# Performance work log

Measured on AMD Instinct MI355X. Metric: run time of the kernel, lower is better.

## Reference

```python
import jax, jax.numpy as jnp
import numpy as np

D, H, L, P, NQ, B, DFF = 256, 8, 4, 4, 900, 4, 1024
SHAPES = [(128, 128), (64, 64), (32, 32), (16, 16)]
S = sum(h * w for h, w in SHAPES)  # 21760
HD = D // H


def setup_inputs() -> dict:
    key = jax.random.key(0)
    ks = iter(jax.random.split(key, 32))
    r = lambda sh, s=1.0: jax.random.normal(next(ks), sh, jnp.float32) * s
    return dict(
        tgt=r((B, NQ, D)),
        query_pos=r((B, NQ, D)),
        reference_points=jax.random.uniform(next(ks), (B, NQ, L, 2), jnp.float32),
        memory=r((B, S, D)),
        in_proj_w=r((D, 3 * D), 0.02), in_proj_b=jnp.zeros(3 * D, jnp.float32),
        out_proj_w=r((D, D), 0.02), out_proj_b=jnp.zeros(D, jnp.float32),
        ln1_g=jnp.ones(D, jnp.float32), ln1_b=jnp.zeros(D, jnp.float32),
        ln2_g=jnp.ones(D, jnp.float32), ln2_b=jnp.zeros(D, jnp.float32),
        ln3_g=jnp.ones(D, jnp.float32), ln3_b=jnp.zeros(D, jnp.float32),
        vproj_w=r((D, D), 0.02), vproj_b=jnp.zeros(D, jnp.float32),
        off_w=r((D, H * L * P * 2), 0.02), off_b=r((H * L * P * 2,), 0.5),
        aw_w=r((D, H * L * P), 0.02), aw_b=jnp.zeros(H * L * P, jnp.float32),
        oproj_w=r((D, D), 0.02), oproj_b=jnp.zeros(D, jnp.float32),
        lin1_w=r((D, DFF), 0.02), lin1_b=jnp.zeros(DFF, jnp.float32),
        lin2_w=r((DFF, D), 0.02), lin2_b=jnp.zeros(D, jnp.float32),
        spatial_shapes=np.array(SHAPES, np.int32),
        mem_mask=jnp.zeros((B, S), bool),
    )


def _ln(x, g, b):
    m = jnp.mean(x, -1, keepdims=True)
    v = jnp.mean((x - m) ** 2, -1, keepdims=True)
    return (x - m) * jax.lax.rsqrt(v + 1e-5) * g + b


def reference(tgt, query_pos, reference_points, memory,
              in_proj_w, in_proj_b, out_proj_w, out_proj_b,
              ln1_g, ln1_b, ln2_g, ln2_b, ln3_g, ln3_b,
              vproj_w, vproj_b, off_w, off_b, aw_w, aw_b, oproj_w, oproj_b,
              lin1_w, lin1_b, lin2_w, lin2_b, spatial_shapes, mem_mask):
    shapes = np.asarray(spatial_shapes)  # static level shapes

    # ---- self attention (nn.MultiheadAttention, q=k=tgt+pos, v=tgt) ----
    qp = tgt + query_pos
    q = qp @ in_proj_w[:, :D] + in_proj_b[:D]
    k = qp @ in_proj_w[:, D:2 * D] + in_proj_b[D:2 * D]
    v = tgt @ in_proj_w[:, 2 * D:] + in_proj_b[2 * D:]
    split = lambda x: x.reshape(B, NQ, H, HD).transpose(0, 2, 1, 3)
    qh, kh, vh = split(q), split(k), split(v)
    att = jax.nn.softmax(jnp.einsum('bhqd,bhkd->bhqk', qh, kh) / np.sqrt(HD).astype(np.float32), -1)
    sa = jnp.einsum('bhqk,bhkd->bhqd', att, vh).transpose(0, 2, 1, 3).reshape(B, NQ, D)
    tgt = _ln(tgt + sa @ out_proj_w + out_proj_b, ln2_g, ln2_b)

    # ---- MSDeformAttn cross attention ----
    query = tgt + query_pos
    value = memory @ vproj_w + vproj_b
    value = jnp.where(mem_mask[..., None], 0.0, value).reshape(B, S, H, HD)
    off = (query @ off_w + off_b).reshape(B, NQ, H, L, P, 2)
    aw = jax.nn.softmax((query @ aw_w + aw_b).reshape(B, NQ, H, L * P), -1).reshape(B, NQ, H, L, P)
    # offset normalizer is (W_l, H_l)
    normalizer = jnp.stack([jnp.asarray(shapes[:, 1]), jnp.asarray(shapes[:, 0])], -1).astype(jnp.float32)
    loc = reference_points[:, :, None, :, None, :] + off / normalizer[None, None, None, :, None, :]

    acc = jnp.zeros((B, NQ, H, HD), tgt.dtype)
    start = 0
    bidx = jnp.arange(B)[:, None, None, None]
    hidx = jnp.arange(H)[None, None, :, None]
    for l in range(L):
        Hl, Wl = int(shapes[l, 0]), int(shapes[l, 1])
        vf = value[:, start:start + Hl * Wl]  # [B, Hl*Wl, H, HD]
        # grid_sample align_corners=False, zero padding: pixel = loc*size - 0.5
        x = loc[:, :, :, l, :, 0] * Wl - 0.5  # [B,NQ,H,P]
        y = loc[:, :, :, l, :, 1] * Hl - 0.5
        x0 = jnp.floor(x); y0 = jnp.floor(y)
        wx = x - x0; wy = y - y0
        x0i = x0.astype(jnp.int32); y0i = y0.astype(jnp.int32)

        def gather(xi, yi):
            valid = (xi >= 0) & (xi < Wl) & (yi >= 0) & (yi < Hl)
            idx = jnp.clip(yi, 0, Hl - 1) * Wl + jnp.clip(xi, 0, Wl - 1)
            g = vf[bidx, idx, hidx]  # [B,NQ,H,P,HD]
            return jnp.where(valid[..., None], g, 0.0)

        samp = (gather(x0i, y0i) * ((1 - wx) * (1 - wy))[..., None]
                + gather(x0i + 1, y0i) * (wx * (1 - wy))[..., None]
                + gather(x0i, y0i + 1) * ((1 - wx) * wy)[..., None]
                + gather(x0i + 1, y0i + 1) * (wx * wy)[..., None])
        acc = acc + (samp * aw[:, :, :, l, :, None]).sum(3)
        start += Hl * Wl

    ca = acc.reshape(B, NQ, D) @ oproj_w + oproj_b
    tgt = _ln(tgt + ca, ln1_g, ln1_b)

    # ---- FFN ----
    ff = jax.nn.relu(tgt @ lin1_w + lin1_b) @ lin2_w + lin2_b
    return _ln(tgt + ff, ln3_g, ln3_b)
```

## Files before the change

### kernel.cpp

```cpp
#include <hip/hip_runtime.h>
#include <hip/hip_bf16.h>

typedef __attribute__((ext_vector_type(8))) short bf16x8;
typedef __attribute__((ext_vector_type(4))) short bf16x4;
typedef __attribute__((ext_vector_type(4))) float f32x4;

#define DEV static __device__ __forceinline__

constexpr int Bc = 4, NQc = 900, Hc = 8, Sc = 21760;
constexpr int M1 = Bc * NQc;
constexpr int NQT = (NQc + 63) / 64;
constexpr int QT16 = (NQc + 15) / 16;
constexpr int QKo = Bc * Hc * 960 * 32;

DEV short f2bf(float f) {
  union { __hip_bfloat16 h; short s; } u;
  u.h = __float2bfloat16(f);
  return u.s;
}
DEV float bf2f(short s) {
  union { short s; __hip_bfloat16 h; } u;
  u.s = s;
  return __bfloat162float(u.h);
}

DEV void pack_body(const float* W, short* Wt, int K, int N, int t) {
  int n = t % N;
  int k4 = (t / N) * 4;
  bf16x4 o;
  o[0] = f2bf(W[(size_t)(k4 + 0) * N + n]);
  o[1] = f2bf(W[(size_t)(k4 + 1) * N + n]);
  o[2] = f2bf(W[(size_t)(k4 + 2) * N + n]);
  o[3] = f2bf(W[(size_t)(k4 + 3) * N + n]);
  *(bf16x4*)&Wt[((size_t)(k4 >> 5) * N + n) * 32 + (k4 & 31)] = o;
}

__global__ __launch_bounds__(256) void pack_all_k(
    const float* w0, short* t0, const float* w1, short* t1,
    const float* w2, short* t2, const float* w3, short* t3,
    const float* w4, short* t4, const float* w5, short* t5) {
  int t = blockIdx.x * 256 + threadIdx.x;
  if (t < 49152) pack_body(w0, t0, 256, 768, t);
  else if (t < 65536) pack_body(w1, t1, 256, 256, t - 49152);
  else if (t < 81920) pack_body(w2, t2, 256, 256, t - 65536);
  else if (t < 98304) pack_body(w3, t3, 256, 256, t - 81920);
  else if (t < 163840) pack_body(w4, t4, 256, 1024, t - 98304);
  else pack_body(w5, t5, 1024, 256, t - 163840);
}

template <int MODE, int ACT, int MT>
__global__ __launch_bounds__(256) void gemmv_k(
    const float* __restrict__ A, const float* __restrict__ A2,
    const short* __restrict__ Wt, const float* __restrict__ bias,
    void* __restrict__ Cv, float* __restrict__ C2, int M, int N, int K,
    const unsigned char* __restrict__ rowmask, const float* __restrict__ g,
    const float* __restrict__ beta, const float* __restrict__ resid,
    const float* __restrict__ qpos, float* __restrict__ out2) {
  constexpr int IT = MT / 16;
  __shared__ short As[MT * 40];
  __shared__ short Ws[256 * 40];
  const int nb = N >> 8;
  const int mb = blockIdx.x / nb, bn = blockIdx.x - mb * nb;
  const int tid = threadIdx.x;
  const int lane = tid & 63, wave = tid >> 6;
  const int l16 = lane & 15, quad = lane >> 4;
  const int sr = (MT == 64) ? (tid >> 2) : (tid >> 3);
  const int sk = (MT == 64) ? ((tid & 3) * 8) : ((tid & 7) * 4);
  const int arow = mb * MT + sr;
  const bool aval = arow < M;
  const bool useA2 = (MODE == 4) ? (bn < 2) : (A2 != nullptr);
  const float* ap = A + (size_t)arow * K + sk;
  const float* ap2 = (A2 ? A2 : A) + (size_t)arow * K + sk;
  const short* wp = Wt + (size_t)(bn * 256 + tid) * 32;
  const size_t wstep = (size_t)N * 32;
  const int KT = K >> 5;

  f32x4 acc[IT][4] = {};
  float4 pa0[2] = {}, pa1[2] = {};
  bf16x8 pw[2][4];

  auto loadA = [&](int s, int it) {
    if (aval) {
      const float* p = ap + it * 32;
      pa0[s] = *(const float4*)p;
      if constexpr (MT == 64) pa1[s] = *(const float4*)(p + 4);
      if (useA2) {
        const float* p2 = ap2 + it * 32;
        float4 q0 = *(const float4*)p2;
        pa0[s].x += q0.x; pa0[s].y += q0.y; pa0[s].z += q0.z; pa0[s].w += q0.w;
        if constexpr (MT == 64) {
          float4 q1 = *(const float4*)(p2 + 4);
          pa1[s].x += q1.x; pa1[s].y += q1.y; pa1[s].z += q1.z; pa1[s].w += q1.w;
        }
      }
    }
  };
  auto loadW = [&](int s, int it) {
    const short* p = wp + (size_t)it * wstep;
    pw[s][0] = *(const bf16x8*)(p + 0);
    pw[s][1] = *(const bf16x8*)(p + 8);
    pw[s][2] = *(const bf16x8*)(p + 16);
    pw[s][3] = *(const bf16x8*)(p + 24);
  };
  auto stage = [&](int s) {
    if constexpr (MT == 64) {
      bf16x8 t;
      t[0] = f2bf(pa0[s].x); t[1] = f2bf(pa0[s].y); t[2] = f2bf(pa0[s].z); t[3] = f2bf(pa0[s].w);
      t[4] = f2bf(pa1[s].x); t[5] = f2bf(pa1[s].y); t[6] = f2bf(pa1[s].z); t[7] = f2bf(pa1[s].w);
      *(bf16x8*)&As[sr * 40 + sk] = t;
    } else {
      bf16x4 t;
      t[0] = f2bf(pa0[s].x); t[1] = f2bf(pa0[s].y); t[2] = f2bf(pa0[s].z); t[3] = f2bf(pa0[s].w);
      *(bf16x4*)&As[sr * 40 + sk] = t;
    }
    short* wd = &Ws[tid * 40];
    *(bf16x8*)(wd + 0) = pw[s][0];
    *(bf16x8*)(wd + 8) = pw[s][1];
    *(bf16x8*)(wd + 16) = pw[s][2];
    *(bf16x8*)(wd + 24) = pw[s][3];
  };
  auto compute = [&]() {
    bf16x8 af[IT], bfr[4];
#pragma unroll
    for (int i = 0; i < IT; i++)
      af[i] = *(const bf16x8*)&As[(i * 16 + l16) * 40 + quad * 8];
#pragma unroll
    for (int j = 0; j < 4; j++)
      bfr[j] = *(const bf16x8*)&Ws[(wave * 64 + j * 16 + l16) * 40 + quad * 8];
#pragma unroll
    for (int i = 0; i < IT; i++)
#pragma unroll
      for (int j = 0; j < 4; j++)
        acc[i][j] = __builtin_amdgcn_mfma_f32_16x16x32_bf16(af[i], bfr[j], acc[i][j], 0, 0, 0);
  };

  loadA(0, 0); loadW(0, 0);
  loadA(1, 1); loadW(1, 1);
  for (int it = 0; it < KT; it += 2) {
    stage(0);
    __syncthreads();
    if (it + 2 < KT) { loadA(0, it + 2); loadW(0, it + 2); }
    compute();
    __syncthreads();
    stage(1);
    __syncthreads();
    if (it + 3 < KT) { loadA(1, it + 3); loadW(1, it + 3); }
    compute();
    __syncthreads();
  }

  if constexpr (MODE == 4) {
    short* base = (short*)Cv;
#pragma unroll
    for (int i = 0; i < IT; i++)
#pragma unroll
      for (int r = 0; r < 4; r++) {
        const int m = mb * MT + i * 16 + quad * 4 + r;
        if (m >= M) continue;
        const int b = m / NQc, q = m - b * NQc;
#pragma unroll
        for (int j = 0; j < 4; j++) {
          const int cl = wave * 64 + j * 16 + l16;
          const float v = acc[i][j][r] + bias[bn * 256 + cl];
          const int h = cl >> 5, ch = cl & 31;
          if (bn == 0) {
            base[((size_t)(b * 8 + h) * 960 + q) * 32 + ch] =
                f2bf(v * 0.17677669529663687f);
          } else if (bn == 1) {
            base[QKo + ((size_t)(b * 8 + h) * 960 + q) * 32 + ch] = f2bf(v);
          } else {
            base[2 * QKo + ((((size_t)(b * 8 + h) * 15 + (q >> 6)) * 32 + ch) * 64 + (q & 63))] = f2bf(v);
          }
        }
      }
  } else if constexpr (MODE == 0) {
#pragma unroll
    for (int i = 0; i < IT; i++)
#pragma unroll
      for (int j = 0; j < 4; j++) {
        const int cl = wave * 64 + j * 16 + l16;
        const int col = bn * 256 + cl;
        const float bb = bias[col];
#pragma unroll
        for (int r = 0; r < 4; r++) {
          const int m = mb * MT + i * 16 + quad * 4 + r;
          if (m < M) {
            float v = acc[i][j][r] + bb;
            if (ACT == 1) v = fmaxf(v, 0.f);
            ((float*)Cv)[(size_t)m * N + col] = v;
          }
        }
      }
  } else {
#pragma unroll
    for (int j = 0; j < 4; j++) {
      const int cl = wave * 64 + j * 16 + l16;
      const float bb = bias[cl];
#pragma unroll
      for (int i = 0; i < IT; i++)
#pragma unroll
        for (int r = 0; r < 4; r++) {
          const int m = mb * MT + i * 16 + quad * 4 + r;
          const float rs = (m < M) ? resid[(size_t)m * 256 + cl] : 0.f;
          acc[i][j][r] += bb + rs;
        }
    }
    float2* pr = (float2*)As;
#pragma unroll
    for (int i = 0; i < IT; i++)
#pragma unroll
      for (int r = 0; r < 4; r++) {
        float s = 0.f, q = 0.f;
#pragma unroll
        for (int j = 0; j < 4; j++) {
          s += acc[i][j][r];
          q += acc[i][j][r] * acc[i][j][r];
        }
#pragma unroll
        for (int d = 1; d < 16; d <<= 1) {
          s += __shfl_xor(s, d);
          q += __shfl_xor(q, d);
        }
        if (l16 == 0) pr[(i * 16 + quad * 4 + r) * 4 + wave] = make_float2(s, q);
      }
    __syncthreads();
#pragma unroll
    for (int i = 0; i < IT; i++)
#pragma unroll
      for (int r = 0; r < 4; r++) {
        const int ml = i * 16 + quad * 4 + r;
        float2 p0 = pr[ml * 4 + 0], p1 = pr[ml * 4 + 1];
        float2 p2 = pr[ml * 4 + 2], p3 = pr[ml * 4 + 3];
        const float sum = p0.x + p1.x + p2.x + p3.x;
        const float sq = p0.y + p1.y + p2.y + p3.y;
        const float mean = sum * (1.f / 256.f);
        const float var = sq * (1.f / 256.f) - mean * mean;
        const float rstd = rsqrtf(var + 1e-5f);
        const int m = mb * MT + ml;
        if (m < M) {
#pragma unroll
          for (int j = 0; j < 4; j++) {
            const int cl = wave * 64 + j * 16 + l16;
            const float o = (acc[i][j][r] - mean) * rstd * g[cl] + beta[cl];
            ((float*)Cv)[(size_t)m * 256 + cl] = o;
            if (out2) out2[(size_t)m * 256 + cl] = o + qpos[(size_t)m * 256 + cl];
          }
        }
      }
  }
}

__global__ __launch_bounds__(256, 4) void gemm_val_k(
    const float* __restrict__ A, const short* __restrict__ Wt,
    const float* __restrict__ bias, short* __restrict__ Cv, int M,
    const unsigned char* __restrict__ rowmask) {
  __shared__ float As[2][64 * 32];
  const int mb = blockIdx.x >> 1, bn = blockIdx.x & 1;
  const int tid = threadIdx.x;
  const int lane = tid & 63, wave = tid >> 6;
  const int l16 = lane & 15, quad = lane >> 4;
  const int wr = wave & 1, wc = wave >> 1;

  const short* wp = Wt + (size_t)(bn * 128 + wc * 64 + l16) * 32 + quad * 8;

  const int srow_lo = lane >> 3;
  const int schunk = ((lane & 7) ^ srow_lo) * 4;
  const float* abase =
      A + (size_t)(mb * 64 + wave * 8 + srow_lo) * 256 + schunk;

  f32x4 acc[2][4] = {};
  bf16x8 pb[2][4];

  auto stage = [&](int buf, int it) {
#pragma unroll
    for (int call = 0; call < 2; ++call) {
      const float* src = abase + (size_t)call * (32 * 256) + it * 32;
      float* dst = &As[buf][(call * 32 + wave * 8) * 32];
      __builtin_amdgcn_global_load_lds(
          (const __attribute__((address_space(1))) void*)src,
          (__attribute__((address_space(3))) void*)dst, 16, 0, 0);
    }
  };
  auto loadB = [&](int s, int it) {
#pragma unroll
    for (int j = 0; j < 4; j++)
      pb[s][j] = *(const bf16x8*)(wp + (size_t)(it * 256 + j * 16) * 32);
  };
  auto compute = [&](int cur) {
    bf16x8 af[2];
#pragma unroll
    for (int i = 0; i < 2; i++) {
      const int row = wr * 32 + i * 16 + l16;
      const int cb = row & 7;
      const float4 a0 =
          *(const float4*)&As[cur][row * 32 + (((quad * 2) ^ cb) << 2)];
      const float4 a1 =
          *(const float4*)&As[cur][row * 32 + (((quad * 2 + 1) ^ cb) << 2)];
      af[i][0] = f2bf(a0.x); af[i][1] = f2bf(a0.y);
      af[i][2] = f2bf(a0.z); af[i][3] = f2bf(a0.w);
      af[i][4] = f2bf(a1.x); af[i][5] = f2bf(a1.y);
      af[i][6] = f2bf(a1.z); af[i][7] = f2bf(a1.w);
    }
#pragma unroll
    for (int i = 0; i < 2; i++)
#pragma unroll
      for (int j = 0; j < 4; j++)
        acc[i][j] = __builtin_amdgcn_mfma_f32_16x16x32_bf16(af[i], pb[cur][j],
                                                            acc[i][j], 0, 0, 0);
  };

  stage(0, 0);
  loadB(0, 0);
  __syncthreads();
  for (int it = 0; it < 8; ++it) {
    const int cur = it & 1;
    if (it + 1 < 8) { stage(cur ^ 1, it + 1); loadB(cur ^ 1, it + 1); }
    compute(cur);
    __syncthreads();
  }

  float bb[4];
#pragma unroll
  for (int j = 0; j < 4; j++) bb[j] = bias[bn * 128 + wc * 64 + j * 16 + l16];
#pragma unroll
  for (int i = 0; i < 2; i++)
#pragma unroll
    for (int r = 0; r < 4; r++) {
      const int m = mb * 64 + wr * 32 + i * 16 + quad * 4 + r;
      const bool mk = rowmask[m] != 0;
#pragma unroll
      for (int j = 0; j < 4; j++) {
        const int cl = bn * 128 + wc * 64 + j * 16 + l16;
        float v = acc[i][j][r] + bb[j];
        if (mk) v = 0.f;
        Cv[(size_t)m * 256 + cl] = f2bf(v);
      }
    }
}

DEV void gemm32_body(const float* __restrict__ A, const float* __restrict__ W,
                     const float* __restrict__ bias, float* __restrict__ C,
                     int M, int N, int K, int bid) {
  __shared__ float Asf[16][64];
  __shared__ float Bsf[16][68];
  const int nb = N >> 6;
  const int bm = bid / nb, bn = bid % nb;
  const int tid = threadIdx.x;
  const int tm = tid >> 4, tn = tid & 15;
  float acc[4][4] = {};

  for (int k0 = 0; k0 < K; k0 += 16) {
    {
      const int m = tid >> 2, kk = (tid & 3) * 4;
      const int row = bm * 64 + m;
      float4 v = (row < M) ? *(const float4*)(A + (size_t)row * K + k0 + kk)
                           : make_float4(0.f, 0.f, 0.f, 0.f);
      Asf[kk + 0][m] = v.x; Asf[kk + 1][m] = v.y;
      Asf[kk + 2][m] = v.z; Asf[kk + 3][m] = v.w;
    }
    {
      const int kk = tid >> 4, n = (tid & 15) * 4;
      float4 v = *(const float4*)(W + (size_t)(k0 + kk) * N + bn * 64 + n);
      *(float4*)&Bsf[kk][n] = v;
    }
    __syncthreads();
#pragma unroll
    for (int kk = 0; kk < 16; kk++) {
      float a[4], b[4];
#pragma unroll
      for (int i = 0; i < 4; i++) a[i] = Asf[kk][tm * 4 + i];
#pragma unroll
      for (int j = 0; j < 4; j++) b[j] = Bsf[kk][tn * 4 + j];
#pragma unroll
      for (int i = 0; i < 4; i++)
#pragma unroll
        for (int j = 0; j < 4; j++) acc[i][j] = fmaf(a[i], b[j], acc[i][j]);
    }
    __syncthreads();
  }
#pragma unroll
  for (int i = 0; i < 4; i++) {
    const int row = bm * 64 + tm * 4 + i;
    if (row >= M) continue;
#pragma unroll
    for (int j = 0; j < 4; j++) {
      const int col = bn * 64 + tn * 4 + j;
      C[(size_t)row * N + col] = acc[i][j] + bias[col];
    }
  }
}

__global__ __launch_bounds__(256) void gemm32_offaw_k(
    const float* __restrict__ query, const float* __restrict__ off_w,
    const float* __restrict__ off_b, float* __restrict__ offb,
    const float* __restrict__ aw_w, const float* __restrict__ aw_b,
    float* __restrict__ awlin) {
  if (blockIdx.x < 228)
    gemm32_body(query, off_w, off_b, offb, M1, 256, 256, blockIdx.x);
  else
    gemm32_body(query, aw_w, aw_b, awlin, M1, 128, 256, blockIdx.x - 228);
}

__global__ __launch_bounds__(128) void attn_k(const short* __restrict__ qbf,
                                              const short* __restrict__ kbf,
                                              const short* __restrict__ vtbf,
                                              float* __restrict__ sa) {
  __shared__ short Pb[2][16 * 72];
  __shared__ float Om[2][16][32];
  __shared__ float Ml[2][16][2];
  const int bid = blockIdx.x;
  const int qt = bid % QT16, bh = bid / QT16;
  const int tid = threadIdx.x, lane = tid & 63, wave = tid >> 6;
  const int l16 = lane & 15, quad = lane >> 4;

  const int q_local = min(qt * 16 + l16, NQc - 1);
  const bf16x8 qf = *(const bf16x8*)&qbf[((size_t)bh * 960 + q_local) * 32 + quad * 8];
  const short* kb = kbf + (size_t)bh * 960 * 32;
  const short* vb = vtbf + (size_t)bh * 15 * 32 * 64;

  f32x4 o0 = {}, o1 = {};
  float mrun[4] = {-1e30f, -1e30f, -1e30f, -1e30f};
  float lrun[4] = {0.f, 0.f, 0.f, 0.f};
  short* pw = Pb[wave];

  for (int kt = wave; kt < NQT; kt += 2) {
    const int k0 = kt * 64;
    f32x4 s[4];
#pragma unroll
    for (int st = 0; st < 4; st++) {
      const int key = k0 + st * 16 + l16;
      const bf16x8 kf = *(const bf16x8*)&kb[(size_t)key * 32 + quad * 8];
      f32x4 z = {};
      s[st] = __builtin_amdgcn_mfma_f32_16x16x32_bf16(qf, kf, z, 0, 0, 0);
      if (key >= NQc) { s[st][0] = -1e30f; s[st][1] = -1e30f; s[st][2] = -1e30f; s[st][3] = -1e30f; }
    }
    float mnew[4], alpha[4];
#pragma unroll
    for (int r = 0; r < 4; r++) {
      float mx = fmaxf(fmaxf(s[0][r], s[1][r]), fmaxf(s[2][r], s[3][r]));
#pragma unroll
      for (int d = 1; d < 16; d <<= 1) mx = fmaxf(mx, __shfl_xor(mx, d));
      mnew[r] = fmaxf(mrun[r], mx);
      alpha[r] = __expf(mrun[r] - mnew[r]);
      mrun[r] = mnew[r];
    }
    float tsum[4] = {0.f, 0.f, 0.f, 0.f};
#pragma unroll
    for (int st = 0; st < 4; st++)
#pragma unroll
      for (int r = 0; r < 4; r++) {
        float p = __expf(s[st][r] - mnew[r]);
        s[st][r] = p;
        tsum[r] += p;
      }
#pragma unroll
    for (int r = 0; r < 4; r++) {
      float t = tsum[r];
#pragma unroll
      for (int d = 1; d < 16; d <<= 1) t += __shfl_xor(t, d);
      lrun[r] = lrun[r] * alpha[r] + t;
      o0[r] *= alpha[r];
      o1[r] *= alpha[r];
    }
#pragma unroll
    for (int st = 0; st < 4; st++)
#pragma unroll
      for (int r = 0; r < 4; r++)
        pw[(quad * 4 + r) * 72 + st * 16 + l16] = f2bf(s[st][r]);
    const short* vt = vb + kt * (32 * 64);
#pragma unroll
    for (int c = 0; c < 2; c++) {
      bf16x8 pf = *(const bf16x8*)&pw[l16 * 72 + c * 32 + quad * 8];
      bf16x8 vf0 = *(const bf16x8*)&vt[(size_t)l16 * 64 + c * 32 + quad * 8];
      bf16x8 vf1 = *(const bf16x8*)&vt[(size_t)(16 + l16) * 64 + c * 32 + quad * 8];
      o0 = __builtin_amdgcn_mfma_f32_16x16x32_bf16(pf, vf0, o0, 0, 0, 0);
      o1 = __builtin_amdgcn_mfma_f32_16x16x32_bf16(pf, vf1, o1, 0, 0, 0);
    }
  }
#pragma unroll
  for (int r = 0; r < 4; r++) {
    Om[wave][quad * 4 + r][l16] = o0[r];
    Om[wave][quad * 4 + r][16 + l16] = o1[r];
  }
  if (l16 == 0) {
#pragma unroll
    for (int r = 0; r < 4; r++) {
      Ml[wave][quad * 4 + r][0] = mrun[r];
      Ml[wave][quad * 4 + r][1] = lrun[r];
    }
  }
  __syncthreads();
  {
    const int q = tid >> 3;
    const int c4 = (tid & 7) * 4;
    const float m0 = Ml[0][q][0], m1 = Ml[1][q][0];
    const float M = fmaxf(m0, m1);
    const float a0 = __expf(m0 - M), a1 = __expf(m1 - M);
    const float lsum = a0 * Ml[0][q][1] + a1 * Ml[1][q][1];
    const int qg = qt * 16 + q;
    if (qg < NQc) {
      const float inv = 1.f / lsum;
      float4 o;
      o.x = (a0 * Om[0][q][c4 + 0] + a1 * Om[1][q][c4 + 0]) * inv;
      o.y = (a0 * Om[0][q][c4 + 1] + a1 * Om[1][q][c4 + 1]) * inv;
      o.z = (a0 * Om[0][q][c4 + 2] + a1 * Om[1][q][c4 + 2]) * inv;
      o.w = (a0 * Om[0][q][c4 + 3] + a1 * Om[1][q][c4 + 3]) * inv;
      const int b = bh >> 3, h = bh & 7;
      *(float4*)&sa[(size_t)(b * NQc + qg) * 256 + h * 32 + c4] = o;
    }
  }
}

__global__ __launch_bounds__(256) void sample_k(
    const float* __restrict__ awlin, const float* __restrict__ off,
    const float* __restrict__ refp, const short* __restrict__ value,
    float* __restrict__ accout) {
  const int wid = blockIdx.x * 4 + (threadIdx.x >> 6);
  const int lane = threadIdx.x & 63;
  const int bq = wid >> 3, h = wid & 7;
  const int b = bq / NQc;
  const int l16 = lane & 15;

  float wraw = awlin[(size_t)bq * 128 + h * 16 + l16];
  float mx = wraw;
#pragma unroll
  for (int d = 1; d < 16; d <<= 1) mx = fmaxf(mx, __shfl_xor(mx, d));
  float e = __expf(wraw - mx), ssum = e;
#pragma unroll
  for (int d = 1; d < 16; d <<= 1) ssum += __shfl_xor(ssum, d);
  const float wnorm = e / ssum;

  const int ch = lane & 31, sub = lane >> 5;
  float facc = 0.f;
#pragma unroll
  for (int it = 0; it < 8; it++) {
    const int pt = it * 2 + sub;
    const float w = __shfl(wnorm, pt);
    const int l = pt >> 2;
    const int W = 128 >> l;
    const int start = (l == 0) ? 0 : (l == 1) ? 16384 : (l == 2) ? 20480 : 21504;
    const float offx = off[(size_t)bq * 256 + h * 32 + pt * 2];
    const float offy = off[(size_t)bq * 256 + h * 32 + pt * 2 + 1];
    const float rx = refp[(size_t)bq * 8 + l * 2];
    const float ry = refp[(size_t)bq * 8 + l * 2 + 1];
    const float x = rx * (float)W + offx - 0.5f;
    const float y = ry * (float)W + offy - 0.5f;
    const float x0f = floorf(x), y0f = floorf(y);
    const float wx = x - x0f, wy = y - y0f;
    const int x0 = (int)x0f, y0 = (int)y0f;
    const short* vbp = value + ((size_t)b * Sc + start) * 256 + h * 32 + ch;
#pragma unroll
    for (int c4 = 0; c4 < 4; c4++) {
      const int dx = c4 & 1, dy = c4 >> 1;
      const int xi = x0 + dx, yi = y0 + dy;
      const bool valid = (xi >= 0) && (xi < W) && (yi >= 0) && (yi < W);
      const int xc = min(max(xi, 0), W - 1);
      const int yc = min(max(yi, 0), W - 1);
      const float gvv = bf2f(vbp[(size_t)(yc * W + xc) * 256]);
      const float ww = (dx ? wx : 1.f - wx) * (dy ? wy : 1.f - wy);
      facc += valid ? w * ww * gvv : 0.f;
    }
  }
  facc += __shfl_xor(facc, 32);
  if (lane < 32) accout[(size_t)bq * 256 + h * 32 + ch] = facc;
}

extern "C" void kernel_launch(void* const* d_in, const int* in_sizes, int n_in,
                              void* d_out, int out_size, void* d_ws,
                              size_t ws_size, hipStream_t stream) {
  const float* tgt = (const float*)d_in[0];
  const float* query_pos = (const float*)d_in[1];
  const float* refp = (const float*)d_in[2];
  const float* memory = (const float*)d_in[3];
  const float* in_proj_w = (const float*)d_in[4];
  const float* in_proj_b = (const float*)d_in[5];
  const float* out_proj_w = (const float*)d_in[6];
  const float* out_proj_b = (const float*)d_in[7];
  const float* ln1_g = (const float*)d_in[8];
  const float* ln1_b = (const float*)d_in[9];
  const float* ln2_g = (const float*)d_in[10];
  const float* ln2_b = (const float*)d_in[11];
  const float* ln3_g = (const float*)d_in[12];
  const float* ln3_b = (const float*)d_in[13];
  const float* vproj_w = (const float*)d_in[14];
  const float* vproj_b = (const float*)d_in[15];
  const float* off_w = (const float*)d_in[16];
  const float* off_b = (const float*)d_in[17];
  const float* aw_w = (const float*)d_in[18];
  const float* aw_b = (const float*)d_in[19];
  const float* oproj_w = (const float*)d_in[20];
  const float* oproj_b = (const float*)d_in[21];
  const float* lin1_w = (const float*)d_in[22];
  const float* lin1_b = (const float*)d_in[23];
  const float* lin2_w = (const float*)d_in[24];
  const float* lin2_b = (const float*)d_in[25];
  const unsigned char* mem_mask = (const unsigned char*)d_in[27];
  float* out = (float*)d_out;

  float* ws = (float*)d_ws;
  short* qbf = (short*)(ws + 921600);
  float* sa = ws + 3686400;
  float* tgt2 = ws + 5529600;
  float* query = ws + 6451200;
  float* offb = ws + 7372800;
  float* awlin = ws + 8294400;
  float* accb = ws + 8755200;
  float* tgt3 = ws + 9676800;
  float* ff1 = ws + 10598400;
  short* valueBf = (short*)(ws + 14284800);
  short* wbase = valueBf + 22282240;
  short* inT = wbase + 0;
  short* outT = wbase + 196608;
  short* vT = wbase + 262144;
  short* oT = wbase + 327680;
  short* lin1T = wbase + 393216;
  short* lin2T = wbase + 655360;

  pack_all_k<<<896, 256, 0, stream>>>(in_proj_w, inT, out_proj_w, outT,
                                      vproj_w, vT, oproj_w, oT,
                                      lin1_w, lin1T, lin2_w, lin2T);

  gemmv_k<4, 0, 32><<<113 * 3, 256, 0, stream>>>(
      tgt, query_pos, inT, in_proj_b, qbf, nullptr, M1, 768, 256,
      nullptr, nullptr, nullptr, nullptr, nullptr, nullptr);
  attn_k<<<Bc * Hc * QT16, 128, 0, stream>>>(qbf, qbf + QKo, qbf + 2 * QKo, sa);
  gemmv_k<3, 0, 32><<<113, 256, 0, stream>>>(
      sa, nullptr, outT, out_proj_b, tgt2, nullptr, M1, 256, 256,
      nullptr, ln2_g, ln2_b, tgt, query_pos, query);
  gemm_val_k<<<2720, 256, 0, stream>>>(memory, vT, vproj_b, valueBf, Bc * Sc, mem_mask);
  gemm32_offaw_k<<<342, 256, 0, stream>>>(query, off_w, off_b, offb, aw_w, aw_b, awlin);
  sample_k<<<Bc * NQc * Hc / 4, 256, 0, stream>>>(awlin, offb, refp, valueBf, accb);
  gemmv_k<3, 0, 32><<<113, 256, 0, stream>>>(
      accb, nullptr, oT, oproj_b, tgt3, nullptr, M1, 256, 256,
      nullptr, ln1_g, ln1_b, tgt2, nullptr, nullptr);
  gemmv_k<0, 1, 64><<<57 * 4, 256, 0, stream>>>(
      tgt3, nullptr, lin1T, lin1_b, ff1, nullptr, M1, 1024, 256,
      nullptr, nullptr, nullptr, nullptr, nullptr, nullptr);
  gemmv_k<3, 0, 32><<<113, 256, 0, stream>>>(
      ff1, nullptr, lin2T, lin2_b, out, nullptr, M1, 256, 1024,
      nullptr, ln3_g, ln3_b, tgt3, nullptr, nullptr);
}
```

Measured before the change: 403.2 us.

## Stage value-projection weights through LDS with a 4-deep async pipeline

The value-projection GEMM now stages the bf16 weight tiles into shared memory with async global-to-LDS loads, alongside the activation tiles, instead of loading them into registers. The double buffer becomes a 4-stage ring with three tiles prefetched. Each step waits on explicit vmcnt counts and uses one barrier per iteration. This is meant to hide global load latency better, at the cost of more LDS per block, a lower occupancy hint, and fragile hand-tuned wait counts.

```diff
diff --git a/kernel.cpp b/kernel.cpp
--- a/kernel.cpp
+++ b/kernel.cpp
@@ -250,52 +250,54 @@
   }
 }
 
-__global__ __launch_bounds__(256, 4) void gemm_val_k(
+__global__ __launch_bounds__(256, 2) void gemm_val_k(
     const float* __restrict__ A, const short* __restrict__ Wt,
     const float* __restrict__ bias, short* __restrict__ Cv, int M,
     const unsigned char* __restrict__ rowmask) {
-  __shared__ float As[2][64 * 32];
+  __shared__ float As[4][64 * 32];
+  __shared__ short Bs[4][128 * 32];
   const int mb = blockIdx.x >> 1, bn = blockIdx.x & 1;
   const int tid = threadIdx.x;
   const int lane = tid & 63, wave = tid >> 6;
   const int l16 = lane & 15, quad = lane >> 4;
   const int wr = wave & 1, wc = wave >> 1;
 
-  const short* wp = Wt + (size_t)(bn * 128 + wc * 64 + l16) * 32 + quad * 8;
-
-  const int srow_lo = lane >> 3;
-  const int schunk = ((lane & 7) ^ srow_lo) * 4;
-  const float* abase =
-      A + (size_t)(mb * 64 + wave * 8 + srow_lo) * 256 + schunk;
+  const int srow = lane >> 3;
+  const int schunk = ((lane & 7) ^ srow) * 4;
+  const float* abase = A + (size_t)(mb * 64 + wave * 8 + srow) * 256 + schunk;
+  const short* bbase =
+      Wt + (size_t)(bn * 128 + wave * 32 + (lane >> 2)) * 32 + (lane & 3) * 8;
 
   f32x4 acc[2][4] = {};
-  bf16x8 pb[2][4];
 
   auto stage = [&](int buf, int it) {
 #pragma unroll
     for (int call = 0; call < 2; ++call) {
-      const float* src = abase + (size_t)call * (32 * 256) + it * 32;
-      float* dst = &As[buf][(call * 32 + wave * 8) * 32];
+      const float* asrc = abase + (size_t)(call * 32) * 256 + it * 32;
+      float* adst = &As[buf][(call * 32 + wave * 8) * 32];
       __builtin_amdgcn_global_load_lds(
-          (const __attribute__((address_space(1))) void*)src,
-          (__attribute__((address_space(3))) void*)dst, 16, 0, 0);
+          (const __attribute__((address_space(1))) void*)asrc,
+          (__attribute__((address_space(3))) void*)adst, 16, 0, 0);
+      const short* bsrc = bbase + ((size_t)it * 256 + call * 16) * 32;
+      short* bdst = &Bs[buf][(wave * 32 + call * 16) * 32];
+      __builtin_amdgcn_global_load_lds(
+          (const __attribute__((address_space(1))) void*)bsrc,
+          (__attribute__((address_space(3))) void*)bdst, 16, 0, 0);
     }
   };
-  auto loadB = [&](int s, int it) {
+  auto compute = [&](int buf) {
+    bf16x8 af[2], bfr[4];
 #pragma unroll
     for (int j = 0; j < 4; j++)
-      pb[s][j] = *(const bf16x8*)(wp + (size_t)(it * 256 + j * 16) * 32);
-  };
-  auto compute = [&](int cur) {
-    bf16x8 af[2];
+      bfr[j] = *(const bf16x8*)&Bs[buf][(wc * 64 + j * 16 + l16) * 32 + quad * 8];
 #pragma unroll
     for (int i = 0; i < 2; i++) {
       const int row = wr * 32 + i * 16 + l16;
       const int cb = row & 7;
       const float4 a0 =
-          *(const float4*)&As[cur][row * 32 + (((quad * 2) ^ cb) << 2)];
+          *(const float4*)&As[buf][row * 32 + (((quad * 2) ^ cb) << 2)];
       const float4 a1 =
-          *(const float4*)&As[cur][row * 32 + (((quad * 2 + 1) ^ cb) << 2)];
+          *(const float4*)&As[buf][row * 32 + (((quad * 2 + 1) ^ cb) << 2)];
       af[i][0] = f2bf(a0.x); af[i][1] = f2bf(a0.y);
       af[i][2] = f2bf(a0.z); af[i][3] = f2bf(a0.w);
       af[i][4] = f2bf(a1.x); af[i][5] = f2bf(a1.y);
@@ -305,19 +307,31 @@
     for (int i = 0; i < 2; i++)
 #pragma unroll
       for (int j = 0; j < 4; j++)
-        acc[i][j] = __builtin_amdgcn_mfma_f32_16x16x32_bf16(af[i], pb[cur][j],
+        acc[i][j] = __builtin_amdgcn_mfma_f32_16x16x32_bf16(af[i], bfr[j],
                                                             acc[i][j], 0, 0, 0);
   };
 
   stage(0, 0);
-  loadB(0, 0);
-  __syncthreads();
-  for (int it = 0; it < 8; ++it) {
-    const int cur = it & 1;
-    if (it + 1 < 8) { stage(cur ^ 1, it + 1); loadB(cur ^ 1, it + 1); }
-    compute(cur);
-    __syncthreads();
-  }
+  stage(1, 1);
+  stage(2, 2);
+
+#define VITER(T, VMSTR)                                     \
+  asm volatile("s_waitcnt vmcnt(" VMSTR ")" ::: "memory");  \
+  __builtin_amdgcn_sched_barrier(0);                        \
+  __builtin_amdgcn_s_barrier();                             \
+  __builtin_amdgcn_sched_barrier(0);                        \
+  if constexpr ((T) + 3 < 8) stage(((T) + 3) & 3, (T) + 3); \
+  compute((T) & 3);
+
+  VITER(0, "8")
+  VITER(1, "8")
+  VITER(2, "8")
+  VITER(3, "8")
+  VITER(4, "8")
+  VITER(5, "8")
+  VITER(6, "4")
+  VITER(7, "0")
+#undef VITER
 
   float bb[4];
 #pragma unroll
```

Result: no change. 407.0 us (+1.0%).

## Make value-projection GEMM persistent with LDS-resident weight half-tile

Applied to the files above, without the earlier changes.

The value projection GEMM now runs as a persistent kernel of 512 blocks. Each block loads its 128-column half of the bf16 weight (64KB) into LDS once, then loops over 128-row tiles. The A operand is read straight from global into registers with a register double buffer, which replaces the old LDS staging through global_load_lds and its per-iteration barriers. This removes repeated weight reloads across 2720 small blocks and the sync overhead, but lowers occupancy (launch bounds 2) and uses uncoalesced strided row reads of A.

```diff
diff --git a/kernel.cpp b/kernel.cpp
--- a/kernel.cpp
+++ b/kernel.cpp
@@ -250,92 +250,84 @@
   }
 }
 
-__global__ __launch_bounds__(256, 4) void gemm_val_k(
+__global__ __launch_bounds__(256, 2) void gemm_val_k(
     const float* __restrict__ A, const short* __restrict__ Wt,
     const float* __restrict__ bias, short* __restrict__ Cv, int M,
     const unsigned char* __restrict__ rowmask) {
-  __shared__ float As[2][64 * 32];
-  const int mb = blockIdx.x >> 1, bn = blockIdx.x & 1;
+  __shared__ short Ws[8 * 128 * 32];
+  const int bid = blockIdx.x;
+  const int bn = bid & 1;
   const int tid = threadIdx.x;
   const int lane = tid & 63, wave = tid >> 6;
   const int l16 = lane & 15, quad = lane >> 4;
-  const int wr = wave & 1, wc = wave >> 1;
-
-  const short* wp = Wt + (size_t)(bn * 128 + wc * 64 + l16) * 32 + quad * 8;
-
-  const int srow_lo = lane >> 3;
-  const int schunk = ((lane & 7) ^ srow_lo) * 4;
-  const float* abase =
-      A + (size_t)(mb * 64 + wave * 8 + srow_lo) * 256 + schunk;
-
-  f32x4 acc[2][4] = {};
-  bf16x8 pb[2][4];
-
-  auto stage = [&](int buf, int it) {
-#pragma unroll
-    for (int call = 0; call < 2; ++call) {
-      const float* src = abase + (size_t)call * (32 * 256) + it * 32;
-      float* dst = &As[buf][(call * 32 + wave * 8) * 32];
-      __builtin_amdgcn_global_load_lds(
-          (const __attribute__((address_space(1))) void*)src,
-          (__attribute__((address_space(3))) void*)dst, 16, 0, 0);
-    }
-  };
-  auto loadB = [&](int s, int it) {
-#pragma unroll
-    for (int j = 0; j < 4; j++)
-      pb[s][j] = *(const bf16x8*)(wp + (size_t)(it * 256 + j * 16) * 32);
-  };
-  auto compute = [&](int cur) {
-    bf16x8 af[2];
+
+#pragma unroll
+  for (int t = 0; t < 16; ++t) {
+    const int id = t * 256 + tid;
+    const int kt = id >> 9, c = id & 511;
+    *(bf16x8*)&Ws[kt * 4096 + c * 8] =
+        *(const bf16x8*)&Wt[((size_t)kt * 256 + bn * 128) * 32 + c * 8];
+  }
+  __syncthreads();
+
+  float bcol[8];
+#pragma unroll
+  for (int j = 0; j < 8; j++) bcol[j] = bias[bn * 128 + j * 16 + l16];
+
+  for (int rt = bid >> 1; rt < 680; rt += 256) {
+    const float* ap =
+        A + ((size_t)rt * 128 + wave * 32 + l16) * 256 + quad * 8;
+    f32x4 acc[2][8] = {};
+    float4 pa[2][2][2];
 #pragma unroll
     for (int i = 0; i < 2; i++) {
-      const int row = wr * 32 + i * 16 + l16;
-      const int cb = row & 7;
-      const float4 a0 =
-          *(const float4*)&As[cur][row * 32 + (((quad * 2) ^ cb) << 2)];
-      const float4 a1 =
-          *(const float4*)&As[cur][row * 32 + (((quad * 2 + 1) ^ cb) << 2)];
-      af[i][0] = f2bf(a0.x); af[i][1] = f2bf(a0.y);
-      af[i][2] = f2bf(a0.z); af[i][3] = f2bf(a0.w);
-      af[i][4] = f2bf(a1.x); af[i][5] = f2bf(a1.y);
-      af[i][6] = f2bf(a1.z); af[i][7] = f2bf(a1.w);
+      pa[0][i][0] = *(const float4*)(ap + i * 16 * 256);
+      pa[0][i][1] = *(const float4*)(ap + i * 16 * 256 + 4);
+    }
+#pragma unroll
+    for (int kt = 0; kt < 8; kt++) {
+      const int cur = kt & 1;
+      if (kt + 1 < 8) {
+#pragma unroll
+        for (int i = 0; i < 2; i++) {
+          pa[cur ^ 1][i][0] =
+              *(const float4*)(ap + i * 16 * 256 + (kt + 1) * 32);
+          pa[cur ^ 1][i][1] =
+              *(const float4*)(ap + i * 16 * 256 + (kt + 1) * 32 + 4);
+        }
+      }
+      bf16x8 af[2];
+#pragma unroll
+      for (int i = 0; i < 2; i++) {
+        af[i][0] = f2bf(pa[cur][i][0].x); af[i][1] = f2bf(pa[cur][i][0].y);
+        af[i][2] = f2bf(pa[cur][i][0].z); af[i][3] = f2bf(pa[cur][i][0].w);
+        af[i][4] = f2bf(pa[cur][i][1].x); af[i][5] = f2bf(pa[cur][i][1].y);
+        af[i][6] = f2bf(pa[cur][i][1].z); af[i][7] = f2bf(pa[cur][i][1].w);
+      }
+#pragma unroll
+      for (int j = 0; j < 8; j++) {
+        const bf16x8 bfr =
+            *(const bf16x8*)&Ws[kt * 4096 + (j * 16 + l16) * 32 + quad * 8];
+#pragma unroll
+        for (int i = 0; i < 2; i++)
+          acc[i][j] = __builtin_amdgcn_mfma_f32_16x16x32_bf16(af[i], bfr,
+                                                              acc[i][j], 0, 0, 0);
+      }
     }
 #pragma unroll
     for (int i = 0; i < 2; i++)
 #pragma unroll
-      for (int j = 0; j < 4; j++)
-        acc[i][j] = __builtin_amdgcn_mfma_f32_16x16x32_bf16(af[i], pb[cur][j],
-                                                            acc[i][j], 0, 0, 0);
-  };
-
-  stage(0, 0);
-  loadB(0, 0);
-  __syncthreads();
-  for (int it = 0; it < 8; ++it) {
-    const int cur = it & 1;
-    if (it + 1 < 8) { stage(cur ^ 1, it + 1); loadB(cur ^ 1, it + 1); }
-    compute(cur);
-    __syncthreads();
-  }
-
-  float bb[4];
-#pragma unroll
-  for (int j = 0; j < 4; j++) bb[j] = bias[bn * 128 + wc * 64 + j * 16 + l16];
-#pragma unroll
-  for (int i = 0; i < 2; i++)
-#pragma unroll
-    for (int r = 0; r < 4; r++) {
-      const int m = mb * 64 + wr * 32 + i * 16 + quad * 4 + r;
-      const bool mk = rowmask[m] != 0;
-#pragma unroll
-      for (int j = 0; j < 4; j++) {
-        const int cl = bn * 128 + wc * 64 + j * 16 + l16;
-        float v = acc[i][j][r] + bb[j];
-        if (mk) v = 0.f;
-        Cv[(size_t)m * 256 + cl] = f2bf(v);
-      }
-    }
+      for (int r = 0; r < 4; r++) {
+        const int m = rt * 128 + wave * 32 + i * 16 + quad * 4 + r;
+        const bool mk = rowmask[m] != 0;
+#pragma unroll
+        for (int j = 0; j < 8; j++) {
+          float v = acc[i][j][r] + bcol[j];
+          if (mk) v = 0.f;
+          Cv[(size_t)m * 256 + bn * 128 + j * 16 + l16] = f2bf(v);
+        }
+      }
+  }
 }
 
 DEV void gemm32_body(const float* __restrict__ A, const float* __restrict__ W,
@@ -627,7 +619,7 @@
   gemmv_k<3, 0, 32><<<113, 256, 0, stream>>>(
       sa, nullptr, outT, out_proj_b, tgt2, nullptr, M1, 256, 256,
       nullptr, ln2_g, ln2_b, tgt, query_pos, query);
-  gemm_val_k<<<2720, 256, 0, stream>>>(memory, vT, vproj_b, valueBf, Bc * Sc, mem_mask);
+  gemm_val_k<<<512, 256, 0, stream>>>(memory, vT, vproj_b, valueBf, Bc * Sc, mem_mask);
   gemm32_offaw_k<<<342, 256, 0, stream>>>(query, off_w, off_b, offb, aw_w, aw_b, awlin);
   sample_k<<<Bc * NQc * Hc / 4, 256, 0, stream>>>(awlin, offb, refp, valueBf, accb);
   gemmv_k<3, 0, 32><<<113, 256, 0, stream>>>(
```

New measurement: 463.3 us. 14.9% more time.
